# Optimization experiments

Hardware: AMD Instinct MI355X
Metric: run time of the kernel (lower is better)

## Reference

```python
import jax, jax.numpy as jnp
import numpy as np

DIM, NHEADS = 1536, 12
HEAD_DIM = DIM // NHEADS  # 128

def _rope_params(max_pos, d):
    inv = 1.0 / (10000.0 ** (np.arange(0, d, 2, dtype=np.float64) / d))
    ang = np.outer(np.arange(max_pos, dtype=np.float64), inv)
    return np.stack([np.cos(ang), np.sin(ang)], -1).astype(np.float32)  # [max_pos, d//2, 2]

def setup_inputs() -> dict:
    key = jax.random.key(0)
    ks = jax.random.split(key, 8)
    B, F, H, W = 1, 3, 30, 52
    L = F * H * W  # 4680
    def w(k):
        return jax.random.normal(k, (DIM, DIM), jnp.float32) * 0.02
    # Wan rope table: head_dim=128 -> segments of real dim 44, 42, 42 (complex 22,21,21)
    freqs = np.concatenate([_rope_params(1024, 44), _rope_params(1024, 42), _rope_params(1024, 42)], axis=1)
    return {
        "x": jax.random.normal(ks[0], (B, L, DIM), jnp.float32),
        "wq": w(ks[1]), "bq": jnp.zeros((DIM,), jnp.float32),
        "wk": w(ks[2]), "bk": jnp.zeros((DIM,), jnp.float32),
        "wv": w(ks[3]), "bv": jnp.zeros((DIM,), jnp.float32),
        "wo": w(ks[4]), "bo": jnp.zeros((DIM,), jnp.float32),
        "gq": jnp.ones((DIM,), jnp.float32),
        "gk": jnp.ones((DIM,), jnp.float32),
        "freqs": jnp.asarray(freqs),                       # [1024, 64, 2] (cos, sin)
        "seq_lens": jnp.array([L], jnp.int64),
        "grid_sizes": jnp.array([[F, H, W]], jnp.int64),
        "F": F, "H": H, "W": W,
        "sink_size": 1, "local_attn_size": 2,
    }

def _rmsnorm(x, g, eps=1e-6):
    xf = x.astype(jnp.float32)
    return xf * jax.lax.rsqrt(jnp.mean(xf * xf, -1, keepdims=True) + eps) * g

def _rope_table(freqs, F, H, W):
    # freqs: [1024, 64, 2]; split complex dims [22, 21, 21] for (t, h, w)
    c = freqs.shape[1]
    s0 = c - 2 * (c // 3)          # 22
    s1 = c // 3                    # 21
    ft = jnp.broadcast_to(freqs[:F, :s0].reshape(F, 1, 1, s0, 2), (F, H, W, s0, 2))
    fh = jnp.broadcast_to(freqs[:H, s0:s0 + s1].reshape(1, H, 1, s1, 2), (F, H, W, s1, 2))
    fw = jnp.broadcast_to(freqs[:W, s0 + s1:].reshape(1, 1, W, s1, 2), (F, H, W, s1, 2))
    return jnp.concatenate([ft, fh, fw], -2).reshape(F * H * W, c, 2)  # [L, c, 2]

def _apply_rope(t, fr):
    # t: [B, L, n, d]; fr: [L, c, 2] with c = d // 2; complex multiply in real arithmetic
    B, L, n, d = t.shape
    c = d // 2
    tr = t.reshape(B, L, n, c, 2)
    a, b = tr[..., 0], tr[..., 1]
    cos = fr[None, :, None, :, 0]
    sin = fr[None, :, None, :, 1]
    out = jnp.stack([a * cos - b * sin, a * sin + b * cos], -1)
    return out.reshape(B, L, n, d)

def reference(x, wq, bq, wk, bk, wv, bv, wo, bo, gq, gk, freqs, seq_lens, grid_sizes,
              F, H, W, sink_size, local_attn_size):
    B, L, dim = x.shape
    n, d = NHEADS, HEAD_DIM
    q = _rmsnorm(x @ wq.T + bq, gq).reshape(B, L, n, d)
    k = _rmsnorm(x @ wk.T + bk, gk).reshape(B, L, n, d)
    v = (x @ wv.T + bv).reshape(B, L, n, d)
    fr = _rope_table(freqs, F, H, W)
    rq = _apply_rope(q, fr)
    rk = _apply_rope(k, fr)
    # sink + causal local-window block mask at frame granularity
    frame = jnp.arange(L) // (H * W)
    fq, fk = frame[:, None], frame[None, :]
    allow = (fk <= fq) & ((fk < sink_size) | (fq - fk < local_attn_size))  # [L, L]
    scores = jnp.einsum('blnd,bmnd->bnlm', rq, rk) / jnp.sqrt(jnp.float32(d))
    scores = jnp.where(allow[None, None], scores, -jnp.inf)
    p = jax.nn.softmax(scores, axis=-1)
    out = jnp.einsum('bnlm,bmnd->blnd', p, v).reshape(B, L, dim)
    return out @ wo.T + bo
```

## Files before the change

kernel.cpp:

```cpp
#include <hip/hip_runtime.h>

#define L_SEQ 4680
#define DIMSZ 1536
#define NHEAD 12
#define HDIM 128
#define FRAME 1560
#define NKT_ALL 74
#define SCALE_L2E 0.12751743f
#define WSZ 2359296
#define XSZ 7274496
#define PMPITCH 4736

typedef float f32x4 __attribute__((ext_vector_type(4)));
typedef _Float16 f16;
typedef _Float16 f16x2 __attribute__((ext_vector_type(2)));
typedef _Float16 f16x4 __attribute__((ext_vector_type(4)));
typedef _Float16 f16x8 __attribute__((ext_vector_type(8)));
typedef unsigned short u16;

__device__ __forceinline__ void gll16(const void* g, void* l) {
  __builtin_amdgcn_global_load_lds(
      (const __attribute__((address_space(1))) unsigned int*)g,
      (__attribute__((address_space(3))) unsigned int*)l, 16, 0, 0);
}

__global__ __launch_bounds__(256) void split_a16(
    const float* __restrict__ A, int R, f16* __restrict__ out) {
  const int rt = blockIdx.x, kt = blockIdx.y;
  const int t = threadIdx.x;
  const int row = t >> 1, c0 = (t & 1) * 16;
  const int gr = min(rt * 128 + row, R - 1);
  const float* src = &A[(size_t)gr * DIMSZ + kt * 32 + c0];
  float f[16];
#pragma unroll
  for (int i = 0; i < 4; ++i) *(float4*)&f[i * 4] = *(const float4*)&src[i * 4];
  size_t obase = ((size_t)(rt * 48 + kt)) * 4096 + row * 32;
#pragma unroll
  for (int cc = 0; cc < 2; ++cc) {
    f16x8 o;
#pragma unroll
    for (int i = 0; i < 8; ++i) o[i] = (f16)f[cc * 8 + i];
    int s = (c0 >> 3) + cc;
    *(f16x8*)&out[obase + ((s * 8) ^ ((row & 3) * 8))] = o;
  }
}

__global__ __launch_bounds__(256) void split_w16h3(
    const float* __restrict__ s0, const float* __restrict__ s1, const float* __restrict__ s2,
    f16* __restrict__ hi_base) {
  const int z = blockIdx.z;
  const float* A = z == 0 ? s0 : (z == 1 ? s1 : s2);
  f16* hi = hi_base + (size_t)z * WSZ;
  const int rt = blockIdx.x, kt = blockIdx.y;
  const int t = threadIdx.x;
  const int row = t >> 1, c0 = (t & 1) * 16;
  const float* src = &A[(size_t)(rt * 128 + row) * DIMSZ + kt * 32 + c0];
  float f[16];
#pragma unroll
  for (int i = 0; i < 4; ++i) *(float4*)&f[i * 4] = *(const float4*)&src[i * 4];
  size_t obase = ((size_t)(rt * 48 + kt)) * 4096 + row * 32;
#pragma unroll
  for (int cc = 0; cc < 2; ++cc) {
    f16x8 oh;
#pragma unroll
    for (int i = 0; i < 8; ++i) oh[i] = (f16)f[cc * 8 + i];
    int s = (c0 >> 3) + cc;
    *(f16x8*)&hi[obase + ((s * 8) ^ ((row & 3) * 8))] = oh;
  }
}

__global__ __launch_bounds__(256) void split_w16(
    const float* __restrict__ A, f16* __restrict__ hi, f16* __restrict__ lo8) {
  const int rt = blockIdx.x, kt = blockIdx.y;
  const int t = threadIdx.x;
  const int row = t >> 1, c0 = (t & 1) * 16;
  const float* src = &A[(size_t)(rt * 128 + row) * DIMSZ + kt * 32 + c0];
  float f[16];
#pragma unroll
  for (int i = 0; i < 4; ++i) *(float4*)&f[i * 4] = *(const float4*)&src[i * 4];
  size_t obase = ((size_t)(rt * 48 + kt)) * 4096 + row * 32;
#pragma unroll
  for (int cc = 0; cc < 2; ++cc) {
    f16x8 oh, ol;
#pragma unroll
    for (int i = 0; i < 8; ++i) {
      float v = f[cc * 8 + i];
      f16 h = (f16)v;
      oh[i] = h;
      ol[i] = (f16)((v - (float)h) * 256.0f);
    }
    int s = (c0 >> 3) + cc;
    size_t off = obase + ((s * 8) ^ ((row & 3) * 8));
    *(f16x8*)&hi[off] = oh;
    *(f16x8*)&lo8[off] = ol;
  }
}

__global__ __launch_bounds__(256, 3) void gemm_f16_1p(
    const f16* __restrict__ A, const f16* __restrict__ Wh,
    const float* __restrict__ b0, const float* __restrict__ b1, const float* __restrict__ b2,
    float* __restrict__ C, int M) {
  __shared__ f16 S[2][2][4096];
  const int t = threadIdx.x;
  const int lane = t & 63, w = t >> 6;
  const int g = lane >> 4, ln = lane & 15;
  const int wm = w >> 1, wn = w & 1;
  const int mt = blockIdx.x, nt = blockIdx.y;
  const int which = nt / 12, ntw = nt - which * 12;
  const float* bias = which == 0 ? b0 : (which == 1 ? b1 : b2);
  const f16* srcs[2] = {A + (size_t)mt * 48 * 4096,
                        Wh + ((size_t)which * 12 + ntw) * 48 * 4096};
  float* Cw = C + (size_t)which * ((size_t)L_SEQ * DIMSZ);
  f32x4 acc[4][4] = {};
#pragma unroll
  for (int a = 0; a < 2; ++a)
#pragma unroll
    for (int i = 0; i < 2; ++i)
      gll16(srcs[a] + (i * 256 + t) * 8, &S[0][a][(i * 256 + t) * 8]);
  int buf = 0;
  for (int kt = 0; kt < 48; ++kt) {
    __syncthreads();
    if (kt + 1 < 48) {
      int b = buf ^ 1;
#pragma unroll
      for (int a = 0; a < 2; ++a)
#pragma unroll
        for (int i = 0; i < 2; ++i)
          gll16(srcs[a] + (size_t)(kt + 1) * 4096 + (i * 256 + t) * 8,
                &S[b][a][(i * 256 + t) * 8]);
    }
    f16x8 af[4], wh4[4];
#pragma unroll
    for (int mi = 0; mi < 4; ++mi) {
      int row = wm * 64 + mi * 16 + ln;
      af[mi] = *(const f16x8*)&S[buf][0][row * 32 + ((g * 8) ^ ((row & 3) * 8))];
    }
#pragma unroll
    for (int ni = 0; ni < 4; ++ni) {
      int row = wn * 64 + ni * 16 + ln;
      wh4[ni] = *(const f16x8*)&S[buf][1][row * 32 + ((g * 8) ^ ((row & 3) * 8))];
    }
#pragma unroll
    for (int mi = 0; mi < 4; ++mi)
#pragma unroll
      for (int ni = 0; ni < 4; ++ni)
        acc[mi][ni] = __builtin_amdgcn_mfma_f32_16x16x32_f16(af[mi], wh4[ni], acc[mi][ni], 0, 0, 0);
    buf ^= 1;
  }
#pragma unroll
  for (int mi = 0; mi < 4; ++mi)
#pragma unroll
    for (int ni = 0; ni < 4; ++ni) {
      int col = ntw * 128 + wn * 64 + ni * 16 + ln;
      float bv = bias[col];
#pragma unroll
      for (int r = 0; r < 4; ++r) {
        int row = mt * 128 + wm * 64 + mi * 16 + 4 * g + r;
        if (row < M) Cw[(size_t)row * DIMSZ + col] = acc[mi][ni][r] + bv;
      }
    }
}

__global__ __launch_bounds__(256, 3) void gemm_f16(
    const f16* __restrict__ A, const f16* __restrict__ Wh, const f16* __restrict__ Wl,
    const float* __restrict__ b0, const float* __restrict__ b1, const float* __restrict__ b2,
    float* __restrict__ C, int M) {
  __shared__ f16 S[2][3][4096];
  const int t = threadIdx.x;
  const int lane = t & 63, w = t >> 6;
  const int g = lane >> 4, ln = lane & 15;
  const int wm = w >> 1, wn = w & 1;
  const int mt = blockIdx.x, nt = blockIdx.y;
  const int which = nt / 12, ntw = nt - which * 12;
  const float* bias = which == 0 ? b0 : (which == 1 ? b1 : b2);
  const f16* srcs[3] = {A + (size_t)mt * 48 * 4096,
                        Wh + ((size_t)which * 12 + ntw) * 48 * 4096,
                        Wl + ((size_t)which * 12 + ntw) * 48 * 4096};
  float* Cw = C + (size_t)which * ((size_t)L_SEQ * DIMSZ);
  f32x4 acc[4][4] = {};
#pragma unroll
  for (int a = 0; a < 3; ++a)
#pragma unroll
    for (int i = 0; i < 2; ++i)
      gll16(srcs[a] + (i * 256 + t) * 8, &S[0][a][(i * 256 + t) * 8]);
  int buf = 0;
  const f16 sc = (f16)0.00390625f;
  for (int kt = 0; kt < 48; ++kt) {
    __syncthreads();
    if (kt + 1 < 48) {
      int b = buf ^ 1;
#pragma unroll
      for (int a = 0; a < 3; ++a)
#pragma unroll
        for (int i = 0; i < 2; ++i)
          gll16(srcs[a] + (size_t)(kt + 1) * 4096 + (i * 256 + t) * 8,
                &S[b][a][(i * 256 + t) * 8]);
    }
    f16x8 af[4], as[4], wh4[4], wl4[4];
#pragma unroll
    for (int mi = 0; mi < 4; ++mi) {
      int row = wm * 64 + mi * 16 + ln;
      int off = row * 32 + ((g * 8) ^ ((row & 3) * 8));
      af[mi] = *(const f16x8*)&S[buf][0][off];
#pragma unroll
      for (int i = 0; i < 8; ++i) as[mi][i] = af[mi][i] * sc;
    }
#pragma unroll
    for (int ni = 0; ni < 4; ++ni) {
      int row = wn * 64 + ni * 16 + ln;
      int off = row * 32 + ((g * 8) ^ ((row & 3) * 8));
      wh4[ni] = *(const f16x8*)&S[buf][1][off];
      wl4[ni] = *(const f16x8*)&S[buf][2][off];
    }
#pragma unroll
    for (int mi = 0; mi < 4; ++mi)
#pragma unroll
      for (int ni = 0; ni < 4; ++ni) {
        acc[mi][ni] = __builtin_amdgcn_mfma_f32_16x16x32_f16(af[mi], wh4[ni], acc[mi][ni], 0, 0, 0);
        acc[mi][ni] = __builtin_amdgcn_mfma_f32_16x16x32_f16(as[mi], wl4[ni], acc[mi][ni], 0, 0, 0);
      }
    buf ^= 1;
  }
#pragma unroll
  for (int mi = 0; mi < 4; ++mi)
#pragma unroll
    for (int ni = 0; ni < 4; ++ni) {
      int col = ntw * 128 + wn * 64 + ni * 16 + ln;
      float bv = bias[col];
#pragma unroll
      for (int r = 0; r < 4; ++r) {
        int row = mt * 128 + wm * 64 + mi * 16 + 4 * g + r;
        if (row < M) Cw[(size_t)row * DIMSZ + col] = acc[mi][ni][r] + bv;
      }
    }
}

__global__ __launch_bounds__(256) void norm_rope(
    const float* __restrict__ qf, const float* __restrict__ kf,
    const float* __restrict__ gq, const float* __restrict__ gk,
    const float* __restrict__ freqs, f16* __restrict__ q16, f16* __restrict__ k16) {
  const int pos = blockIdx.x;
  const bool isq = blockIdx.y == 0;
  const float* row = (isq ? qf : kf) + (size_t)pos * DIMSZ;
  const float* g = isq ? gq : gk;
  const int t = threadIdx.x;
  float2 ab[3];
  float ss = 0.f;
#pragma unroll
  for (int i = 0; i < 3; ++i) {
    ab[i] = *(const float2*)&row[2 * (t + 256 * i)];
    ss += ab[i].x * ab[i].x + ab[i].y * ab[i].y;
  }
#pragma unroll
  for (int m = 32; m; m >>= 1) ss += __shfl_xor(ss, m);
  __shared__ float part[4];
  if ((t & 63) == 0) part[t >> 6] = ss;
  __syncthreads();
  const float tot = part[0] + part[1] + part[2] + part[3];
  float scale = rsqrtf(tot * (1.f / DIMSZ) + 1e-6f);
  if (isq) scale *= SCALE_L2E;
  const int f = pos / FRAME;
  const int rem = pos - f * FRAME;
  const int hh = rem / 52;
  const int ww = rem - hh * 52;
  const int kt = pos >> 6, kk = pos & 63;
#pragma unroll
  for (int i = 0; i < 3; ++i) {
    const int p = t + 256 * i;
    const int c = p & 63;
    const int h = p >> 6;
    const int pr = c < 22 ? f : (c < 43 ? hh : ww);
    const float cs = freqs[(pr * 64 + c) * 2 + 0];
    const float sn = freqs[(pr * 64 + c) * 2 + 1];
    const float a = ab[i].x * scale * g[2 * p];
    const float b = ab[i].y * scale * g[2 * p + 1];
    f16x2 o;
    o[0] = (f16)(a * cs - b * sn);
    o[1] = (f16)(a * sn + b * cs);
    if (isq) {
      *(f16x2*)&q16[(size_t)pos * DIMSZ + 2 * p] = o;
    } else {
      const int s = c >> 2;
      size_t base = ((size_t)(h * NKT_ALL + kt)) << 13;
      *(f16x2*)&k16[base + kk * 128 + ((s * 8) ^ ((kk & 7) * 8)) + (c & 3) * 2] = o;
    }
  }
}

__global__ __launch_bounds__(256) void vconvert(const float* __restrict__ v, f16* __restrict__ v16) {
  __shared__ f16 Ls[64][136];
  const int kt = blockIdx.x, h = blockIdx.y, t = threadIdx.x;
#pragma unroll
  for (int p = 0; p < 8; ++p) {
    int e = p * 1024 + t * 4;
    int kk = e >> 7, d = e & 127;
    int gr = kt * 64 + kk;
    float4 val = make_float4(0.f, 0.f, 0.f, 0.f);
    if (gr < L_SEQ) val = *(const float4*)&v[(size_t)gr * DIMSZ + h * HDIM + d];
    f16x4 o;
    o[0] = (f16)val.x; o[1] = (f16)val.y; o[2] = (f16)val.z; o[3] = (f16)val.w;
    *(f16x4*)&Ls[kk][d] = o;
  }
  __syncthreads();
  f16* out = v16 + (((size_t)(h * NKT_ALL + kt)) << 13);
#pragma unroll
  for (int p = 0; p < 4; ++p) {
    int idx = p * 256 + t;
    int d = idx >> 3, c = idx & 7;
    const int nbb = (c & 1) * 2;
    const int g4 = (c >> 1) * 4;
    f16x8 o;
#pragma unroll
    for (int i = 0; i < 8; ++i) o[i] = Ls[(nbb + (i >> 2)) * 16 + g4 + (i & 3)][d];
    *(f16x8*)&out[d * 64 + 8 * (c ^ (d & 7))] = o;
  }
}

__global__ __launch_bounds__(256, 2) void attn_split(
    const f16* __restrict__ q16, const f16* __restrict__ k16,
    const f16* __restrict__ v16, float* __restrict__ pO,
    float* __restrict__ pm, float* __restrict__ pl) {
  __shared__ f16 Ks[2][8192];
  __shared__ f16 Vt[8192];
  __shared__ float Os[4][16][20];
  const int b = blockIdx.x;
  const int qt = 36 - b / 24;
  const int rem = b % 24;
  const int s = rem / 12;
  const int h = rem % 12;
  const int q0 = qt * 128;
  const int t = threadIdx.x;
  const int lane = t & 63, w = t >> 6;
  const int g = lane >> 4, ln = lane & 15;

  f16x8 qa[2][4];
  int klim[2];
  float m_run[2], l_run[2];
#pragma unroll
  for (int mi = 0; mi < 2; ++mi) {
    int qrow = min(q0 + w * 32 + mi * 16 + ln, L_SEQ - 1);
    klim[mi] = (qrow / FRAME + 1) * FRAME;
    m_run[mi] = -1e30f;
    l_run[mi] = 0.f;
    const f16* qb = &q16[(size_t)qrow * DIMSZ + h * HDIM + g * 8];
#pragma unroll
    for (int kc = 0; kc < 4; ++kc) qa[mi][kc] = *(const f16x8*)&qb[kc * 32];
  }
  const int klim0 = __shfl(klim[0], 0);
  f32x4 acc[2][8] = {};

  const int rmax = min(q0 + 127, L_SEQ - 1);
  const int nkt = ((rmax / FRAME + 1) * FRAME + 63) >> 6;
  const size_t hbase = ((size_t)h * NKT_ALL) << 13;

  f16x8 vv0, vv1, vv2, vv3;
  {
    const f16* tv = v16 + hbase + ((size_t)s << 13) + t * 8;
    vv0 = *(const f16x8*)(tv);
    vv1 = *(const f16x8*)(tv + 2048);
    vv2 = *(const f16x8*)(tv + 4096);
    vv3 = *(const f16x8*)(tv + 6144);
    f16* lv = Vt + t * 8;
    *(f16x8*)(lv) = vv0;
    *(f16x8*)(lv + 2048) = vv1;
    *(f16x8*)(lv + 4096) = vv2;
    *(f16x8*)(lv + 6144) = vv3;
    const f16* tk = k16 + hbase + ((size_t)s << 13);
#pragma unroll
    for (int i = 0; i < 4; ++i) gll16(tk + (i * 256 + t) * 8, &Ks[0][(i * 256 + t) * 8]);
  }
  int cur = 0;
  for (int kt = s; kt < nkt; kt += 2) {
    __syncthreads();
    const bool more = (kt + 2 < nkt);
    if (more) {
      size_t tb = hbase + ((size_t)(kt + 2) << 13);
      const f16* tk = k16 + tb;
#pragma unroll
      for (int i = 0; i < 4; ++i) gll16(tk + (i * 256 + t) * 8, &Ks[cur ^ 1][(i * 256 + t) * 8]);
      const f16* tv = v16 + tb + t * 8;
      vv0 = *(const f16x8*)(tv);
      vv1 = *(const f16x8*)(tv + 2048);
      vv2 = *(const f16x8*)(tv + 4096);
      vv3 = *(const f16x8*)(tv + 6144);
    }
    const f16* Kb = Ks[cur];

    f32x4 st[2][4] = {};
    __builtin_amdgcn_s_setprio(1);
#pragma unroll
    for (int nb = 0; nb < 4; ++nb) {
      int row = nb * 16 + ln;
#pragma unroll
      for (int kc = 0; kc < 4; ++kc) {
        f16x8 kb = *(const f16x8*)&Kb[row * 128 + ((g * 8 + kc * 32) ^ ((row & 7) * 8))];
        st[0][nb] = __builtin_amdgcn_mfma_f32_16x16x32_f16(kb, qa[0][kc], st[0][nb], 0, 0, 0);
        st[1][nb] = __builtin_amdgcn_mfma_f32_16x16x32_f16(kb, qa[1][kc], st[1][nb], 0, 0, 0);
      }
    }
    __builtin_amdgcn_s_setprio(0);

    f16x4 pb[2][4];
    const bool boundary = (kt * 64 + 64 > klim0);
#pragma unroll
    for (int mi = 0; mi < 2; ++mi) {
      float rm = -1e30f;
      if (boundary) {
#pragma unroll
        for (int nb = 0; nb < 4; ++nb)
#pragma unroll
          for (int r = 0; r < 4; ++r) {
            int key = kt * 64 + nb * 16 + 4 * g + r;
            float val = st[mi][nb][r];
            if (key >= klim[mi]) val = -1e30f;
            st[mi][nb][r] = val;
            rm = fmaxf(rm, val);
          }
      } else {
#pragma unroll
        for (int nb = 0; nb < 4; ++nb)
#pragma unroll
          for (int r = 0; r < 4; ++r) rm = fmaxf(rm, st[mi][nb][r]);
      }
      rm = fmaxf(rm, __shfl_xor(rm, 16));
      rm = fmaxf(rm, __shfl_xor(rm, 32));
      if (!__all(rm - m_run[mi] <= 8.0f)) {
        float mn = fmaxf(m_run[mi], rm);
        float fs = exp2f(m_run[mi] - mn);
        m_run[mi] = mn;
        l_run[mi] *= fs;
#pragma unroll
        for (int db = 0; db < 8; ++db)
#pragma unroll
          for (int r = 0; r < 4; ++r) acc[mi][db][r] *= fs;
      }
      float sm = 0.f;
#pragma unroll
      for (int nb = 0; nb < 4; ++nb)
#pragma unroll
        for (int r = 0; r < 4; ++r) {
          float e = exp2f(st[mi][nb][r] - m_run[mi]);
          sm += e;
          pb[mi][nb][r] = (f16)e;
        }
      sm += __shfl_xor(sm, 16);
      sm += __shfl_xor(sm, 32);
      l_run[mi] += sm;
    }

    __builtin_amdgcn_s_setprio(1);
#pragma unroll
    for (int db = 0; db < 8; ++db) {
      int d = db * 16 + ln;
#pragma unroll
      for (int nbp = 0; nbp < 2; ++nbp) {
        f16x8 vvv = *(const f16x8*)&Vt[d * 64 + 8 * ((g * 2 + nbp) ^ (d & 7))];
        f16x4 vlo = {vvv[0], vvv[1], vvv[2], vvv[3]};
        f16x4 vhi = {vvv[4], vvv[5], vvv[6], vvv[7]};
        acc[0][db] = __builtin_amdgcn_mfma_f32_16x16x16f16(vlo, pb[0][2 * nbp], acc[0][db], 0, 0, 0);
        acc[1][db] = __builtin_amdgcn_mfma_f32_16x16x16f16(vlo, pb[1][2 * nbp], acc[1][db], 0, 0, 0);
        acc[0][db] = __builtin_amdgcn_mfma_f32_16x16x16f16(vhi, pb[0][2 * nbp + 1], acc[0][db], 0, 0, 0);
        acc[1][db] = __builtin_amdgcn_mfma_f32_16x16x16f16(vhi, pb[1][2 * nbp + 1], acc[1][db], 0, 0, 0);
      }
    }
    __builtin_amdgcn_s_setprio(0);

    __syncthreads();
    if (more) {
      f16* lv = Vt + t * 8;
      *(f16x8*)(lv) = vv0;
      *(f16x8*)(lv + 2048) = vv1;
      *(f16x8*)(lv + 4096) = vv2;
      *(f16x8*)(lv + 6144) = vv3;
    }
    cur ^= 1;
  }

#pragma unroll
  for (int mi = 0; mi < 2; ++mi) {
    int qrow = q0 + w * 32 + mi * 16 + ln;
    if (g == 0) {
      pm[((size_t)s * 12 + h) * PMPITCH + qrow] = m_run[mi];
      pl[((size_t)s * 12 + h) * PMPITCH + qrow] = l_run[mi];
    }
#pragma unroll
    for (int db = 0; db < 8; ++db) {
      *(f32x4*)&Os[w][ln][4 * g] = acc[mi][db];
      asm volatile("s_waitcnt lgkmcnt(0)" ::: "memory");
#pragma unroll
      for (int r = 0; r < 4; ++r) {
        int q = q0 + w * 32 + mi * 16 + 4 * g + r;
        float val = Os[w][4 * g + r][ln];
        if (q < L_SEQ)
          pO[((size_t)s * L_SEQ + q) * DIMSZ + h * HDIM + db * 16 + ln] = val;
      }
      asm volatile("s_waitcnt lgkmcnt(0)" ::: "memory");
    }
  }
}

__global__ __launch_bounds__(256) void combine_k(
    const float* __restrict__ pO, const float* __restrict__ pm,
    const float* __restrict__ pl, f16* __restrict__ aos) {
  const int qt = blockIdx.x, h = blockIdx.y, t = threadIdx.x;
  const int row = t >> 1, d0 = (t & 1) * 64;
  const int q = min(qt * 128 + row, L_SEQ - 1);
  const float m0 = pm[(size_t)h * PMPITCH + q];
  const float m1 = pm[((size_t)12 + h) * PMPITCH + q];
  const float l0 = pl[(size_t)h * PMPITCH + q];
  const float l1 = pl[((size_t)12 + h) * PMPITCH + q];
  const float m = fmaxf(m0, m1);
  float w0 = exp2f(m0 - m), w1 = exp2f(m1 - m);
  const float rinv = 1.f / (w0 * l0 + w1 * l1);
  w0 *= rinv; w1 *= rinv;
  const float* o0 = &pO[(size_t)q * DIMSZ + h * HDIM + d0];
  const float* o1 = &pO[((size_t)L_SEQ + q) * DIMSZ + h * HDIM + d0];
  f16* outbase = aos + ((size_t)qt * 48 + h * 4) * 4096 + row * 32;
#pragma unroll
  for (int c8 = 0; c8 < 8; ++c8) {
    float a[8], bvals[8];
    *(float4*)&a[0] = *(const float4*)&o0[c8 * 8];
    *(float4*)&a[4] = *(const float4*)&o0[c8 * 8 + 4];
    *(float4*)&bvals[0] = *(const float4*)&o1[c8 * 8];
    *(float4*)&bvals[4] = *(const float4*)&o1[c8 * 8 + 4];
    f16x8 ov;
#pragma unroll
    for (int i = 0; i < 8; ++i) ov[i] = (f16)(w0 * a[i] + w1 * bvals[i]);
    int d = d0 + c8 * 8;
    int ktb = d >> 5;
    int s8 = (d & 31) >> 3;
    *(f16x8*)&outbase[(size_t)ktb * 4096 + ((s8 * 8) ^ ((row & 3) * 8))] = ov;
  }
}

extern "C" void kernel_launch(void* const* d_in, const int* in_sizes, int n_in,
                              void* d_out, int out_size, void* d_ws, size_t ws_size,
                              hipStream_t stream) {
  const float* x  = (const float*)d_in[0];
  const float* wq = (const float*)d_in[1];
  const float* bq = (const float*)d_in[2];
  const float* wk = (const float*)d_in[3];
  const float* bk = (const float*)d_in[4];
  const float* wv = (const float*)d_in[5];
  const float* bv = (const float*)d_in[6];
  const float* wo = (const float*)d_in[7];
  const float* bo = (const float*)d_in[8];
  const float* gq = (const float*)d_in[9];
  const float* gk = (const float*)d_in[10];
  const float* freqs = (const float*)d_in[11];
  float* out = (float*)d_out;
  float* ws = (float*)d_ws;

  const size_t LD = (size_t)L_SEQ * DIMSZ;

  float* qf = ws;
  float* kf = ws + LD;
  float* vf = ws + 2 * LD;
  f16* xs  = (f16*)(ws + 3 * LD);
  f16* k16 = xs + XSZ;
  f16* v16 = k16 + XSZ;
  f16* whi = v16 + XSZ;
  f16* wlo = whi + 3 * (size_t)WSZ;
  f16* q16 = xs;
  float* pO = qf;
  f16* aos = (f16*)vf;
  float* pm = vf + XSZ / 2;
  float* pl = pm + 2 * 12 * PMPITCH;
  f16* wo_hi = (f16*)(pl + 2 * 12 * PMPITCH);
  f16* wo_lo = wo_hi + (size_t)WSZ;
  (void)wlo;

  dim3 blk(256);
  split_a16<<<dim3(37, 48), blk, 0, stream>>>(x, L_SEQ, xs);
  split_w16h3<<<dim3(12, 48, 3), blk, 0, stream>>>(wq, wk, wv, whi);
  gemm_f16_1p<<<dim3(37, 36), blk, 0, stream>>>(xs, whi, bq, bk, bv, qf, L_SEQ);
  norm_rope<<<dim3(L_SEQ, 2), blk, 0, stream>>>(qf, kf, gq, gk, freqs, q16, k16);
  vconvert<<<dim3(NKT_ALL, NHEAD), blk, 0, stream>>>(vf, v16);
  split_w16<<<dim3(12, 48), blk, 0, stream>>>(wo, wo_hi, wo_lo);
  attn_split<<<dim3(37 * 24), blk, 0, stream>>>(q16, k16, v16, pO, pm, pl);
  combine_k<<<dim3(37, 12), blk, 0, stream>>>(pO, pm, pl, aos);
  gemm_f16<<<dim3(37, 12), blk, 0, stream>>>(aos, wo_hi, wo_lo, bo, bo, bo, out, L_SEQ);
}
```

Baseline: 396.4 us.

## Widen QKV GEMM tile to 256 columns and drop lo-part in output GEMM

Replaces the QKV projection GEMM with a 128x256 tile kernel that stages two weight tiles per step and raises MFMA wave priority, halving the number of blocks and improving A-tile reuse. The output projection no longer uses the hi/lo split of Wo: it converts Wo to a single fp16 copy and runs the single-pass GEMM, removing half the MFMAs and the lo-weight traffic. The risk is lower accuracy in the output projection, plus higher register pressure and lower occupancy in the wider tile.

Measured after the change: 384.2 us. 1.03x faster.

```diff
diff --git a/kernel.cpp b/kernel.cpp
--- a/kernel.cpp
+++ b/kernel.cpp
@@ -66,33 +66,6 @@
     for (int i = 0; i < 8; ++i) oh[i] = (f16)f[cc * 8 + i];
     int s = (c0 >> 3) + cc;
     *(f16x8*)&hi[obase + ((s * 8) ^ ((row & 3) * 8))] = oh;
-  }
-}
-
-__global__ __launch_bounds__(256) void split_w16(
-    const float* __restrict__ A, f16* __restrict__ hi, f16* __restrict__ lo8) {
-  const int rt = blockIdx.x, kt = blockIdx.y;
-  const int t = threadIdx.x;
-  const int row = t >> 1, c0 = (t & 1) * 16;
-  const float* src = &A[(size_t)(rt * 128 + row) * DIMSZ + kt * 32 + c0];
-  float f[16];
-#pragma unroll
-  for (int i = 0; i < 4; ++i) *(float4*)&f[i * 4] = *(const float4*)&src[i * 4];
-  size_t obase = ((size_t)(rt * 48 + kt)) * 4096 + row * 32;
-#pragma unroll
-  for (int cc = 0; cc < 2; ++cc) {
-    f16x8 oh, ol;
-#pragma unroll
-    for (int i = 0; i < 8; ++i) {
-      float v = f[cc * 8 + i];
-      f16 h = (f16)v;
-      oh[i] = h;
-      ol[i] = (f16)((v - (float)h) * 256.0f);
-    }
-    int s = (c0 >> 3) + cc;
-    size_t off = obase + ((s * 8) ^ ((row & 3) * 8));
-    *(f16x8*)&hi[off] = oh;
-    *(f16x8*)&lo8[off] = ol;
   }
 }
 
@@ -161,71 +134,69 @@
     }
 }
 
-__global__ __launch_bounds__(256, 3) void gemm_f16(
-    const f16* __restrict__ A, const f16* __restrict__ Wh, const f16* __restrict__ Wl,
+__global__ __launch_bounds__(256, 2) void gemm_w256(
+    const f16* __restrict__ A, const f16* __restrict__ Wh,
     const float* __restrict__ b0, const float* __restrict__ b1, const float* __restrict__ b2,
     float* __restrict__ C, int M) {
-  __shared__ f16 S[2][3][4096];
+  __shared__ f16 SA[2][4096];
+  __shared__ f16 SW[2][8192];
   const int t = threadIdx.x;
   const int lane = t & 63, w = t >> 6;
   const int g = lane >> 4, ln = lane & 15;
   const int wm = w >> 1, wn = w & 1;
   const int mt = blockIdx.x, nt = blockIdx.y;
-  const int which = nt / 12, ntw = nt - which * 12;
+  const int which = nt / 6, ntw = nt - which * 6;
   const float* bias = which == 0 ? b0 : (which == 1 ? b1 : b2);
-  const f16* srcs[3] = {A + (size_t)mt * 48 * 4096,
-                        Wh + ((size_t)which * 12 + ntw) * 48 * 4096,
-                        Wl + ((size_t)which * 12 + ntw) * 48 * 4096};
+  const f16* srcA = A + (size_t)mt * 48 * 4096;
+  const f16* srcW0 = Wh + (size_t)which * WSZ + (size_t)(2 * ntw) * 48 * 4096;
+  const f16* srcW1 = srcW0 + (size_t)48 * 4096;
   float* Cw = C + (size_t)which * ((size_t)L_SEQ * DIMSZ);
-  f32x4 acc[4][4] = {};
-#pragma unroll
-  for (int a = 0; a < 3; ++a)
-#pragma unroll
-    for (int i = 0; i < 2; ++i)
-      gll16(srcs[a] + (i * 256 + t) * 8, &S[0][a][(i * 256 + t) * 8]);
+  f32x4 acc[4][8] = {};
+#pragma unroll
+  for (int i = 0; i < 2; ++i) {
+    gll16(srcA + (i * 256 + t) * 8, &SA[0][(i * 256 + t) * 8]);
+    gll16(srcW0 + (i * 256 + t) * 8, &SW[0][(i * 256 + t) * 8]);
+    gll16(srcW1 + (i * 256 + t) * 8, &SW[0][4096 + (i * 256 + t) * 8]);
+  }
   int buf = 0;
-  const f16 sc = (f16)0.00390625f;
   for (int kt = 0; kt < 48; ++kt) {
     __syncthreads();
     if (kt + 1 < 48) {
       int b = buf ^ 1;
-#pragma unroll
-      for (int a = 0; a < 3; ++a)
-#pragma unroll
-        for (int i = 0; i < 2; ++i)
-          gll16(srcs[a] + (size_t)(kt + 1) * 4096 + (i * 256 + t) * 8,
-                &S[b][a][(i * 256 + t) * 8]);
-    }
-    f16x8 af[4], as[4], wh4[4], wl4[4];
+      size_t ko = (size_t)(kt + 1) * 4096;
+#pragma unroll
+      for (int i = 0; i < 2; ++i) {
+        gll16(srcA + ko + (i * 256 + t) * 8, &SA[b][(i * 256 + t) * 8]);
+        gll16(srcW0 + ko + (i * 256 + t) * 8, &SW[b][(i * 256 + t) * 8]);
+        gll16(srcW1 + ko + (i * 256 + t) * 8, &SW[b][4096 + (i * 256 + t) * 8]);
+      }
+    }
+    f16x8 af[4], wh[8];
 #pragma unroll
     for (int mi = 0; mi < 4; ++mi) {
       int row = wm * 64 + mi * 16 + ln;
-      int off = row * 32 + ((g * 8) ^ ((row & 3) * 8));
-      af[mi] = *(const f16x8*)&S[buf][0][off];
-#pragma unroll
-      for (int i = 0; i < 8; ++i) as[mi][i] = af[mi][i] * sc;
-    }
-#pragma unroll
-    for (int ni = 0; ni < 4; ++ni) {
-      int row = wn * 64 + ni * 16 + ln;
-      int off = row * 32 + ((g * 8) ^ ((row & 3) * 8));
-      wh4[ni] = *(const f16x8*)&S[buf][1][off];
-      wl4[ni] = *(const f16x8*)&S[buf][2][off];
-    }
+      af[mi] = *(const f16x8*)&SA[buf][row * 32 + ((g * 8) ^ ((row & 3) * 8))];
+    }
+#pragma unroll
+    for (int ni = 0; ni < 8; ++ni) {
+      int r = wn * 128 + ni * 16 + ln;
+      int off = (r >> 7) * 4096 + (r & 127) * 32 + ((g * 8) ^ ((r & 3) * 8));
+      wh[ni] = *(const f16x8*)&SW[buf][off];
+    }
+    __builtin_amdgcn_s_setprio(1);
 #pragma unroll
     for (int mi = 0; mi < 4; ++mi)
 #pragma unroll
-      for (int ni = 0; ni < 4; ++ni) {
-        acc[mi][ni] = __builtin_amdgcn_mfma_f32_16x16x32_f16(af[mi], wh4[ni], acc[mi][ni], 0, 0, 0);
-        acc[mi][ni] = __builtin_amdgcn_mfma_f32_16x16x32_f16(as[mi], wl4[ni], acc[mi][ni], 0, 0, 0);
-      }
+      for (int ni = 0; ni < 8; ++ni)
+        acc[mi][ni] = __builtin_amdgcn_mfma_f32_16x16x32_f16(af[mi], wh[ni], acc[mi][ni], 0, 0, 0);
+    __builtin_amdgcn_s_setprio(0);
     buf ^= 1;
   }
 #pragma unroll
   for (int mi = 0; mi < 4; ++mi)
 #pragma unroll
-    for (int ni = 0; ni < 4; ++ni) {
-      int col = ntw * 128 + wn * 64 + ni * 16 + ln;
+    for (int ni = 0; ni < 8; ++ni) {
+      int col = ntw * 256 + wn * 128 + ni * 16 + ln;
       float bv = bias[col];
 #pragma unroll
       for (int r = 0; r < 4; ++r) {
@@ -560,24 +531,21 @@
   f16* k16 = xs + XSZ;
   f16* v16 = k16 + XSZ;
   f16* whi = v16 + XSZ;
-  f16* wlo = whi + 3 * (size_t)WSZ;
   f16* q16 = xs;
   float* pO = qf;
   f16* aos = (f16*)vf;
   float* pm = vf + XSZ / 2;
   float* pl = pm + 2 * 12 * PMPITCH;
   f16* wo_hi = (f16*)(pl + 2 * 12 * PMPITCH);
-  f16* wo_lo = wo_hi + (size_t)WSZ;
-  (void)wlo;
 
   dim3 blk(256);
   split_a16<<<dim3(37, 48), blk, 0, stream>>>(x, L_SEQ, xs);
   split_w16h3<<<dim3(12, 48, 3), blk, 0, stream>>>(wq, wk, wv, whi);
-  gemm_f16_1p<<<dim3(37, 36), blk, 0, stream>>>(xs, whi, bq, bk, bv, qf, L_SEQ);
+  gemm_w256<<<dim3(37, 18), blk, 0, stream>>>(xs, whi, bq, bk, bv, qf, L_SEQ);
   norm_rope<<<dim3(L_SEQ, 2), blk, 0, stream>>>(qf, kf, gq, gk, freqs, q16, k16);
   vconvert<<<dim3(NKT_ALL, NHEAD), blk, 0, stream>>>(vf, v16);
-  split_w16<<<dim3(12, 48), blk, 0, stream>>>(wo, wo_hi, wo_lo);
+  split_w16h3<<<dim3(12, 48, 1), blk, 0, stream>>>(wo, wo, wo, wo_hi);
   attn_split<<<dim3(37 * 24), blk, 0, stream>>>(q16, k16, v16, pO, pm, pl);
   combine_k<<<dim3(37, 12), blk, 0, stream>>>(pO, pm, pl, aos);
-  gemm_f16<<<dim3(37, 12), blk, 0, stream>>>(aos, wo_hi, wo_lo, bo, bo, bo, out, L_SEQ);
-}
+  gemm_f16_1p<<<dim3(37, 12), blk, 0, stream>>>(aos, wo_hi, bo, bo, bo, out, L_SEQ);
+}
```
